# Kernel optimization log

Hardware: AMD Instinct MI355X
Metric: run time of the kernel (lower is better)

Reference implementation:

```python
import jax, jax.numpy as jnp
import numpy as np

T, B, DICO, EMB, LAT = 256, 64, 8192, 256, 256


def setup_inputs() -> dict:
    key = jax.random.key(0)
    ks = jax.random.split(key, 7)
    s_emb = 1.0 / np.sqrt(DICO)
    s_enc = 1.0 / np.sqrt(EMB + LAT)
    return {
        "x": jax.random.normal(ks[0], (T, B, DICO), dtype=jnp.float32),
        "h": jax.random.normal(ks[1], (B, LAT), dtype=jnp.float32),
        "W_emb": jax.random.uniform(ks[2], (DICO, EMB), jnp.float32, -s_emb, s_emb),
        "b_emb": jax.random.uniform(ks[3], (EMB,), jnp.float32, -s_emb, s_emb),
        "W_enc": jax.random.uniform(ks[4], (EMB + LAT, LAT), jnp.float32, -s_enc, s_enc),
        "b_enc": jax.random.uniform(ks[5], (LAT,), jnp.float32, -s_enc, s_enc),
    }


def reference(x, h, W_emb, b_emb, W_enc, b_enc):
    # embedding: [T,B,DICO] @ [DICO,EMB] -> [T,B,EMB]
    xe = jnp.einsum('tbd,de->tbe', x, W_emb) + b_emb
    # split encoder weight into x-part and h-part: cat(x,h)@W == x@Wx + h@Wh
    Wx, Wh = W_enc[:EMB], W_enc[EMB:]
    # hoist the per-step x projection out of the scan (no h dependence)
    xp = jnp.einsum('tbe,el->tbl', xe, Wx) + b_enc  # [T,B,LAT]

    def step(h, xp_t):
        h_new = jnp.tanh(xp_t + h @ Wh)
        return h_new, h_new

    _, hs = jax.lax.scan(step, h, xp)
    return hs  # [T,B,LAT]
```

## Files before the change

### kernel.cpp

```cpp
#include <hip/hip_runtime.h>
#include <hip/hip_bf16.h>
#include <stdint.h>

#define T_DIM 256
#define B_DIM 64
#define DICO  8192
#define EMB   256
#define LAT   256
#define M_DIM (T_DIM*B_DIM)

#define BM 64
#define BN 256
#define BK 64
#define KSPLIT 2
#define KCHUNK (DICO/KSPLIT)
#define NKS (KCHUNK/BK)

typedef short  bf16x8 __attribute__((ext_vector_type(8)));
typedef float  f32x4  __attribute__((ext_vector_type(4)));
typedef _Float16 f16x2 __attribute__((ext_vector_type(2)));

__device__ __forceinline__ ushort f2bf(float f) {
  uint32_t u = __float_as_uint(f);
  u += 0x7FFFu + ((u >> 16) & 1u);
  return (ushort)(u >> 16);
}

__device__ __forceinline__ void glds16(const void* g, void* l) {
  __builtin_amdgcn_global_load_lds(
      (const __attribute__((address_space(1))) uint32_t*)g,
      (__attribute__((address_space(3))) uint32_t*)l, 16, 0, 0);
}

__global__ void wct_kernel(const float* __restrict__ Wemb, const float* __restrict__ Wenc,
                           ushort* __restrict__ wct) {
  const int n  = threadIdx.x;
  const int d0 = blockIdx.x * 32;
  __shared__ float we[32 * 256];
  __shared__ float tr[32 * 257];
  #pragma unroll
  for (int r = 0; r < 32; ++r) we[r*256 + n] = Wemb[(size_t)(d0 + r)*EMB + n];
  __syncthreads();
  float acc[32];
  #pragma unroll
  for (int d = 0; d < 32; ++d) acc[d] = 0.f;
  #pragma unroll 4
  for (int e = 0; e < 256; ++e) {
    float wv = Wenc[e*LAT + n];
    #pragma unroll
    for (int d = 0; d < 32; ++d) acc[d] += we[d*256 + e] * wv;
  }
  #pragma unroll
  for (int d = 0; d < 32; ++d) tr[d*257 + n] = acc[d];
  __syncthreads();
  const int nn0 = n >> 2, kc = n & 3;
  #pragma unroll
  for (int p = 0; p < 4; ++p) {
    int nn = p*64 + nn0;
    bf16x8 v;
    #pragma unroll
    for (int j = 0; j < 8; ++j) v[j] = (short)f2bf(tr[(kc*8 + j)*257 + nn]);
    *(bf16x8*)(wct + (size_t)nn*DICO + d0 + kc*8) = v;
  }
}

__global__ void __launch_bounds__(256, 2) gemm_kernel(const float* __restrict__ x,
                                                      const ushort* __restrict__ wct,
                                                      float* __restrict__ xp) {
  __shared__ __align__(16) ushort sA[2][BM * BK];
  __shared__ __align__(16) ushort sB[2][BN * BK];
  const int tid = threadIdx.x;
  const int bid = blockIdx.x;
  const int swzb = (bid & 7) * 64 + (bid >> 3);
  const int mt = swzb & 255, ksp = swzb >> 8;
  const size_t rowbase = (size_t)mt * BM;
  const int kbase = ksp * KCHUNK;

  const int lane = tid & 63, wid = tid >> 6;
  const int l15 = lane & 15, lc = lane >> 4;

  const int r0 = tid >> 2, c0 = tid & 3;
  const float* ag = x + (rowbase + r0) * (size_t)DICO + kbase + c0 * 16;
  const int sx0 = (((2*c0    ) ^ (r0 & 7)) * 16);
  const int sx1 = (((2*c0 + 1) ^ (r0 & 7)) * 16);

  const int sw0 = (((    lc) ^ (l15 & 7)) * 16);
  const int sw1 = (((4 + lc) ^ (l15 & 7)) * 16);

  const char* wb = (const char*)wct;
  const size_t kb2 = (size_t)kbase * 2;

  const int brow_s = (tid >> 3);
  const int bslot_s = tid & 7;

  f32x4 acc[4][4];
  #pragma unroll
  for (int m = 0; m < 4; ++m)
    #pragma unroll
    for (int n = 0; n < 4; ++n) acc[m][n] = (f32x4){0.f, 0.f, 0.f, 0.f};

  float4 avP[4], avQ[4];

  auto stageB = [&](int buf, int kofs) {
    #pragma unroll
    for (int r = 0; r < 8; ++r) {
      const int row = r * 32 + brow_s;
      const int srcslot = bslot_s ^ (row & 7);
      glds16(wb + (size_t)row * (DICO * 2) + kb2 + (size_t)kofs * 2 + srcslot * 16,
             (char*)&sB[buf][0] + r * 4096 + tid * 16);
    }
  };
  auto storeA = [&](int buf, const float4* av) {
    const float4 a0 = av[0], a1 = av[1], a2 = av[2], a3 = av[3];
    bf16x8 w0, w1;
    w0[0]=(short)f2bf(a0.x); w0[1]=(short)f2bf(a0.y); w0[2]=(short)f2bf(a0.z); w0[3]=(short)f2bf(a0.w);
    w0[4]=(short)f2bf(a1.x); w0[5]=(short)f2bf(a1.y); w0[6]=(short)f2bf(a1.z); w0[7]=(short)f2bf(a1.w);
    w1[0]=(short)f2bf(a2.x); w1[1]=(short)f2bf(a2.y); w1[2]=(short)f2bf(a2.z); w1[3]=(short)f2bf(a2.w);
    w1[4]=(short)f2bf(a3.x); w1[5]=(short)f2bf(a3.y); w1[6]=(short)f2bf(a3.z); w1[7]=(short)f2bf(a3.w);
    char* base = (char*)&sA[buf][0] + r0 * 128;
    *(bf16x8*)(base + sx0) = w0;
    *(bf16x8*)(base + sx1) = w1;
  };
  auto compute = [&](int buf) {
    bf16x8 bfr[4][2];
    #pragma unroll
    for (int n = 0; n < 4; ++n) {
      const char* bb = (const char*)&sB[buf][0] + (wid*64 + n*16 + l15) * 128;
      bfr[n][0] = *(const bf16x8*)(bb + sw0);
      bfr[n][1] = *(const bf16x8*)(bb + sw1);
    }
    #pragma unroll
    for (int m = 0; m < 4; ++m) {
      const char* ab = (const char*)&sA[buf][0] + (m*16 + l15) * 128;
      bf16x8 a0 = *(const bf16x8*)(ab + sw0);
      bf16x8 a1 = *(const bf16x8*)(ab + sw1);
      #pragma unroll
      for (int n = 0; n < 4; ++n) {
        acc[m][n] = __builtin_amdgcn_mfma_f32_16x16x32_bf16(a0, bfr[n][0], acc[m][n], 0, 0, 0);
        acc[m][n] = __builtin_amdgcn_mfma_f32_16x16x32_bf16(a1, bfr[n][1], acc[m][n], 0, 0, 0);
      }
    }
  };

  auto body = [&](int k, float4* avC, float4* avL) {
    const int p = k & 1;
    const int kB = (k + 1 < NKS ? k + 1 : NKS - 1) * BK;
    const int kA = (k + 2 < NKS ? k + 2 : NKS - 1) * BK;
    stageB(p ^ 1, kB);
    asm volatile("" ::: "memory");
    #pragma unroll
    for (int q = 0; q < 4; ++q) avL[q] = *(const float4*)(ag + kA + q * 4);
    storeA(p ^ 1, avC);
    compute(p);
    asm volatile("s_waitcnt vmcnt(4)" ::: "memory");
    asm volatile("s_waitcnt lgkmcnt(0)" ::: "memory");
    __builtin_amdgcn_s_barrier();
    __builtin_amdgcn_sched_barrier(0);
  };

  stageB(0, 0);
  #pragma unroll
  for (int q = 0; q < 4; ++q) avP[q] = *(const float4*)(ag + 0   + q * 4);
  #pragma unroll
  for (int q = 0; q < 4; ++q) avQ[q] = *(const float4*)(ag + BK  + q * 4);
  storeA(0, avP);
  __syncthreads();

  for (int k = 0; k < NKS; k += 2) {
    body(k,     avQ, avP);
    body(k + 1, avP, avQ);
  }

  float* xpo = xp + ((size_t)ksp * M_DIM + rowbase) * LAT;
  #pragma unroll
  for (int m = 0; m < 4; ++m)
    #pragma unroll
    for (int n = 0; n < 4; ++n)
      #pragma unroll
      for (int j = 0; j < 4; ++j)
        xpo[(size_t)(m*16 + lc*4 + j) * LAT + wid*64 + n*16 + l15] = acc[m][n][j];
}

__global__ void __launch_bounds__(256, 1) rnn_kernel(const float* __restrict__ xp,
                           const float* __restrict__ h0, const float* __restrict__ Wenc,
                           const float* __restrict__ bemb, const float* __restrict__ benc,
                           float* __restrict__ out) {
  const int b = blockIdx.x, l = threadIdx.x;
  __shared__ __align__(16) uint32_t hbuf[2][128];
  float bc = benc[l];
  #pragma unroll 8
  for (int e = 0; e < 256; ++e) bc += bemb[e] * Wenc[e*LAT + l];
  f16x2 wh[128];
  #pragma unroll
  for (int j = 0; j < 128; ++j) {
    f16x2 w;
    w[0] = (_Float16)Wenc[(size_t)(EMB + 2*j    )*LAT + l];
    w[1] = (_Float16)Wenc[(size_t)(EMB + 2*j + 1)*LAT + l];
    wh[j] = w;
  }
  ((_Float16*)&hbuf[0][0])[l] = (_Float16)h0[(size_t)b*LAT + l];
  __syncthreads();
  const float* xpb = xp + (size_t)b*LAT + l;
  float*       ob  = out + (size_t)b*LAT + l;
  const size_t ST = (size_t)B_DIM * LAT;
  const size_t PO = (size_t)M_DIM * LAT;
  float xa0 = xpb[0],  xa1 = xpb[PO];
  float xb0 = xpb[ST], xb1 = xpb[ST + PO];
  float xc0 = 0.f, xc1 = 0.f;
  for (int t = 0; t < T_DIM; ++t) {
    if (t + 2 < T_DIM) {
      size_t ni = (size_t)(t + 2) * ST;
      xc0 = xpb[ni]; xc1 = xpb[ni + PO];
    }
    const uint32_t* hc = &hbuf[t & 1][0];
    float s0=0.f,s1=0.f,s2=0.f,s3=0.f,s4=0.f,s5=0.f,s6=0.f,s7=0.f;
    #pragma unroll
    for (int q = 0; q < 16; ++q) {
      uint4 hv0 = *(const uint4*)(hc + q*8);
      uint4 hv1 = *(const uint4*)(hc + q*8 + 4);
      s0 = __builtin_amdgcn_fdot2(wh[q*8+0], __builtin_bit_cast(f16x2, hv0.x), s0, false);
      s1 = __builtin_amdgcn_fdot2(wh[q*8+1], __builtin_bit_cast(f16x2, hv0.y), s1, false);
      s2 = __builtin_amdgcn_fdot2(wh[q*8+2], __builtin_bit_cast(f16x2, hv0.z), s2, false);
      s3 = __builtin_amdgcn_fdot2(wh[q*8+3], __builtin_bit_cast(f16x2, hv0.w), s3, false);
      s4 = __builtin_amdgcn_fdot2(wh[q*8+4], __builtin_bit_cast(f16x2, hv1.x), s4, false);
      s5 = __builtin_amdgcn_fdot2(wh[q*8+5], __builtin_bit_cast(f16x2, hv1.y), s5, false);
      s6 = __builtin_amdgcn_fdot2(wh[q*8+6], __builtin_bit_cast(f16x2, hv1.z), s6, false);
      s7 = __builtin_amdgcn_fdot2(wh[q*8+7], __builtin_bit_cast(f16x2, hv1.w), s7, false);
    }
    float pre = (xa0 + xa1) + bc + (((s0+s1)+(s2+s3)) + ((s4+s5)+(s6+s7)));
    float ax = fabsf(pre);
    float e2 = __expf(-2.f * ax);
    float r  = __fdividef(1.f - e2, 1.f + e2);
    float hn = (pre < 0.f) ? -r : r;
    ob[(size_t)t * ST] = hn;
    ((_Float16*)&hbuf[(t + 1) & 1][0])[l] = (_Float16)hn;
    __builtin_amdgcn_sched_barrier(0);
    asm volatile("s_waitcnt lgkmcnt(0)" ::: "memory");
    __builtin_amdgcn_s_barrier();
    __builtin_amdgcn_sched_barrier(0);
    xa0 = xb0; xa1 = xb1; xb0 = xc0; xb1 = xc1;
  }
}

extern "C" void kernel_launch(void* const* d_in, const int* in_sizes, int n_in,
                              void* d_out, int out_size, void* d_ws, size_t ws_size,
                              hipStream_t stream) {
  const float* x    = (const float*)d_in[0];
  const float* h0   = (const float*)d_in[1];
  const float* Wemb = (const float*)d_in[2];
  const float* bemb = (const float*)d_in[3];
  const float* Wenc = (const float*)d_in[4];
  const float* benc = (const float*)d_in[5];
  float* out = (float*)d_out;

  ushort* wct = (ushort*)d_ws;
  float*  xp  = (float*)((char*)d_ws + ((size_t)4 << 20));

  wct_kernel<<<256, 256, 0, stream>>>(Wemb, Wenc, wct);
  gemm_kernel<<<512, 256, 0, stream>>>(x, wct, xp);
  rnn_kernel<<<64, 256, 0, stream>>>(xp, h0, Wenc, bemb, benc, out);
}
```

Before: 658.9 us.

## Retile GEMM to 128x128 and move RNN recurrence onto MFMA

The input GEMM now uses 128x128 tiles with a 2x2 wave grid in place of 64x256, and converts fp32 to bf16 with the packed v_cvt_pk_bf16_f32 instruction. The recurrent kernel now computes 16 batch rows per block with fp16 MFMA instead of per-thread fdot2 dot products, running 4 blocks of 512 threads instead of 64 blocks. The RNN step becomes cheaper per block but uses far fewer CUs, so its latency depends on how serial steps run. The GEMM retiling changes how much of the x and weight data each tile reuses.

```diff
diff --git a/kernel.cpp b/kernel.cpp
--- a/kernel.cpp
+++ b/kernel.cpp
@@ -9,8 +9,6 @@
 #define LAT   256
 #define M_DIM (T_DIM*B_DIM)
 
-#define BM 64
-#define BN 256
 #define BK 64
 #define KSPLIT 2
 #define KCHUNK (DICO/KSPLIT)
@@ -18,12 +16,18 @@
 
 typedef short  bf16x8 __attribute__((ext_vector_type(8)));
 typedef float  f32x4  __attribute__((ext_vector_type(4)));
-typedef _Float16 f16x2 __attribute__((ext_vector_type(2)));
+typedef _Float16 f16x8 __attribute__((ext_vector_type(8)));
 
 __device__ __forceinline__ ushort f2bf(float f) {
   uint32_t u = __float_as_uint(f);
   u += 0x7FFFu + ((u >> 16) & 1u);
   return (ushort)(u >> 16);
+}
+
+__device__ __forceinline__ uint32_t cvtpk(float lo, float hi) {
+  uint32_t r;
+  asm("v_cvt_pk_bf16_f32 %0, %1, %2" : "=v"(r) : "v"(lo), "v"(hi));
+  return r;
 }
 
 __device__ __forceinline__ void glds16(const void* g, void* l) {
@@ -64,34 +68,36 @@
   }
 }
 
-__global__ void __launch_bounds__(256, 2) gemm_kernel(const float* __restrict__ x,
-                                                      const ushort* __restrict__ wct,
-                                                      float* __restrict__ xp) {
-  __shared__ __align__(16) ushort sA[2][BM * BK];
-  __shared__ __align__(16) ushort sB[2][BN * BK];
+__global__ void __launch_bounds__(256, 2) gemm2_kernel(const float* __restrict__ x,
+                                                       const ushort* __restrict__ wct,
+                                                       float* __restrict__ xp) {
+  __shared__ __align__(16) ushort sA[2][128 * 64];
+  __shared__ __align__(16) ushort sB[2][128 * 64];
   const int tid = threadIdx.x;
   const int bid = blockIdx.x;
   const int swzb = (bid & 7) * 64 + (bid >> 3);
-  const int mt = swzb & 255, ksp = swzb >> 8;
-  const size_t rowbase = (size_t)mt * BM;
+  const int mt  = swzb & 127;
+  const int nt  = (swzb >> 7) & 1;
+  const int ksp = swzb >> 8;
+  const size_t rowbase = (size_t)mt * 128;
   const int kbase = ksp * KCHUNK;
 
   const int lane = tid & 63, wid = tid >> 6;
   const int l15 = lane & 15, lc = lane >> 4;
-
-  const int r0 = tid >> 2, c0 = tid & 3;
-  const float* ag = x + (rowbase + r0) * (size_t)DICO + kbase + c0 * 16;
-  const int sx0 = (((2*c0    ) ^ (r0 & 7)) * 16);
-  const int sx1 = (((2*c0 + 1) ^ (r0 & 7)) * 16);
+  const int wr = wid >> 1, wc = wid & 1;
+
+  const int ar = tid >> 4, ac = tid & 15;
+  const float* ag = x + (rowbase + ar) * (size_t)DICO + kbase + ac * 4;
+  const int awb = (((ac >> 1) ^ (ar & 7)) * 16) + (ac & 1) * 8;
 
   const int sw0 = (((    lc) ^ (l15 & 7)) * 16);
   const int sw1 = (((4 + lc) ^ (l15 & 7)) * 16);
 
   const char* wb = (const char*)wct;
   const size_t kb2 = (size_t)kbase * 2;
-
-  const int brow_s = (tid >> 3);
-  const int bslot_s = tid & 7;
+  const int nrow0 = nt * 128;
+
+  const int brow_s = tid >> 3, bslot_s = tid & 7;
 
   f32x4 acc[4][4];
   #pragma unroll
@@ -99,39 +105,42 @@
     #pragma unroll
     for (int n = 0; n < 4; ++n) acc[m][n] = (f32x4){0.f, 0.f, 0.f, 0.f};
 
-  float4 avP[4], avQ[4];
-
+  float4 avP[8], avQ[8];
+
+  auto loadA = [&](float4* av, int kofs) {
+    #pragma unroll
+    for (int p = 0; p < 8; ++p)
+      av[p] = *(const float4*)(ag + (size_t)(p * 16) * DICO + kofs);
+  };
   auto stageB = [&](int buf, int kofs) {
     #pragma unroll
-    for (int r = 0; r < 8; ++r) {
+    for (int r = 0; r < 4; ++r) {
       const int row = r * 32 + brow_s;
       const int srcslot = bslot_s ^ (row & 7);
-      glds16(wb + (size_t)row * (DICO * 2) + kb2 + (size_t)kofs * 2 + srcslot * 16,
+      glds16(wb + (size_t)(nrow0 + row) * (DICO * 2) + kb2 + (size_t)kofs * 2 + srcslot * 16,
              (char*)&sB[buf][0] + r * 4096 + tid * 16);
     }
   };
   auto storeA = [&](int buf, const float4* av) {
-    const float4 a0 = av[0], a1 = av[1], a2 = av[2], a3 = av[3];
-    bf16x8 w0, w1;
-    w0[0]=(short)f2bf(a0.x); w0[1]=(short)f2bf(a0.y); w0[2]=(short)f2bf(a0.z); w0[3]=(short)f2bf(a0.w);
-    w0[4]=(short)f2bf(a1.x); w0[5]=(short)f2bf(a1.y); w0[6]=(short)f2bf(a1.z); w0[7]=(short)f2bf(a1.w);
-    w1[0]=(short)f2bf(a2.x); w1[1]=(short)f2bf(a2.y); w1[2]=(short)f2bf(a2.z); w1[3]=(short)f2bf(a2.w);
-    w1[4]=(short)f2bf(a3.x); w1[5]=(short)f2bf(a3.y); w1[6]=(short)f2bf(a3.z); w1[7]=(short)f2bf(a3.w);
-    char* base = (char*)&sA[buf][0] + r0 * 128;
-    *(bf16x8*)(base + sx0) = w0;
-    *(bf16x8*)(base + sx1) = w1;
+    #pragma unroll
+    for (int p = 0; p < 8; ++p) {
+      uint2 d;
+      d.x = cvtpk(av[p].x, av[p].y);
+      d.y = cvtpk(av[p].z, av[p].w);
+      *(uint2*)((char*)&sA[buf][0] + (p * 16 + ar) * 128 + awb) = d;
+    }
   };
   auto compute = [&](int buf) {
     bf16x8 bfr[4][2];
     #pragma unroll
     for (int n = 0; n < 4; ++n) {
-      const char* bb = (const char*)&sB[buf][0] + (wid*64 + n*16 + l15) * 128;
+      const char* bb = (const char*)&sB[buf][0] + (wc*64 + n*16 + l15) * 128;
       bfr[n][0] = *(const bf16x8*)(bb + sw0);
       bfr[n][1] = *(const bf16x8*)(bb + sw1);
     }
     #pragma unroll
     for (int m = 0; m < 4; ++m) {
-      const char* ab = (const char*)&sA[buf][0] + (m*16 + l15) * 128;
+      const char* ab = (const char*)&sA[buf][0] + (wr*64 + m*16 + l15) * 128;
       bf16x8 a0 = *(const bf16x8*)(ab + sw0);
       bf16x8 a1 = *(const bf16x8*)(ab + sw1);
       #pragma unroll
@@ -148,21 +157,21 @@
     const int kA = (k + 2 < NKS ? k + 2 : NKS - 1) * BK;
     stageB(p ^ 1, kB);
     asm volatile("" ::: "memory");
-    #pragma unroll
-    for (int q = 0; q < 4; ++q) avL[q] = *(const float4*)(ag + kA + q * 4);
+    loadA(avL, kA);
+    asm volatile("" ::: "memory");
     storeA(p ^ 1, avC);
     compute(p);
-    asm volatile("s_waitcnt vmcnt(4)" ::: "memory");
+    asm volatile("s_waitcnt vmcnt(8)" ::: "memory");
     asm volatile("s_waitcnt lgkmcnt(0)" ::: "memory");
     __builtin_amdgcn_s_barrier();
     __builtin_amdgcn_sched_barrier(0);
   };
 
   stageB(0, 0);
-  #pragma unroll
-  for (int q = 0; q < 4; ++q) avP[q] = *(const float4*)(ag + 0   + q * 4);
-  #pragma unroll
-  for (int q = 0; q < 4; ++q) avQ[q] = *(const float4*)(ag + BK  + q * 4);
+  asm volatile("" ::: "memory");
+  loadA(avP, 0);
+  asm volatile("" ::: "memory");
+  loadA(avQ, BK);
   storeA(0, avP);
   __syncthreads();
 
@@ -171,74 +180,107 @@
     body(k + 1, avP, avQ);
   }
 
-  float* xpo = xp + ((size_t)ksp * M_DIM + rowbase) * LAT;
+  float* xpo = xp + ((size_t)ksp * M_DIM + rowbase) * LAT + nrow0;
   #pragma unroll
   for (int m = 0; m < 4; ++m)
     #pragma unroll
     for (int n = 0; n < 4; ++n)
       #pragma unroll
       for (int j = 0; j < 4; ++j)
-        xpo[(size_t)(m*16 + lc*4 + j) * LAT + wid*64 + n*16 + l15] = acc[m][n][j];
-}
-
-__global__ void __launch_bounds__(256, 1) rnn_kernel(const float* __restrict__ xp,
+        xpo[(size_t)(wr*64 + m*16 + lc*4 + j) * LAT + wc*64 + n*16 + l15] = acc[m][n][j];
+}
+
+__global__ void __launch_bounds__(512, 2) rnn_mfma_kernel(const float* __restrict__ xp,
                            const float* __restrict__ h0, const float* __restrict__ Wenc,
                            const float* __restrict__ bemb, const float* __restrict__ benc,
                            float* __restrict__ out) {
-  const int b = blockIdx.x, l = threadIdx.x;
-  __shared__ __align__(16) uint32_t hbuf[2][128];
-  float bc = benc[l];
-  #pragma unroll 8
-  for (int e = 0; e < 256; ++e) bc += bemb[e] * Wenc[e*LAT + l];
-  f16x2 wh[128];
-  #pragma unroll
-  for (int j = 0; j < 128; ++j) {
-    f16x2 w;
-    w[0] = (_Float16)Wenc[(size_t)(EMB + 2*j    )*LAT + l];
-    w[1] = (_Float16)Wenc[(size_t)(EMB + 2*j + 1)*LAT + l];
-    wh[j] = w;
-  }
-  ((_Float16*)&hbuf[0][0])[l] = (_Float16)h0[(size_t)b*LAT + l];
+  const int tid = threadIdx.x;
+  const int w = tid >> 6, lane = tid & 63;
+  const int l15 = lane & 15, lc = lane >> 4;
+  const int bb = blockIdx.x * 16;
+  const int c0 = w*32 + l15, c1 = c0 + 16;
+  const int rb = lc * 4;
+
+  __shared__ _Float16 hbuf[2][16 * 264];
+
+  f16x8 whf0[8], whf1[8];
+  #pragma unroll
+  for (int ks = 0; ks < 8; ++ks) {
+    f16x8 w0, w1;
+    #pragma unroll
+    for (int j = 0; j < 8; ++j) {
+      const int k = ks*32 + lc*8 + j;
+      w0[j] = (_Float16)Wenc[(size_t)(EMB + k)*LAT + c0];
+      w1[j] = (_Float16)Wenc[(size_t)(EMB + k)*LAT + c1];
+    }
+    whf0[ks] = w0; whf1[ks] = w1;
+  }
+  float bc0 = benc[c0], bc1 = benc[c1];
+  for (int e = 0; e < 256; ++e) {
+    float be = bemb[e];
+    bc0 += be * Wenc[(size_t)e*LAT + c0];
+    bc1 += be * Wenc[(size_t)e*LAT + c1];
+  }
+  #pragma unroll
+  for (int j = 0; j < 4; ++j) {
+    hbuf[0][(rb + j)*264 + c0] = (_Float16)h0[(size_t)(bb + rb + j)*LAT + c0];
+    hbuf[0][(rb + j)*264 + c1] = (_Float16)h0[(size_t)(bb + rb + j)*LAT + c1];
+  }
   __syncthreads();
-  const float* xpb = xp + (size_t)b*LAT + l;
-  float*       ob  = out + (size_t)b*LAT + l;
-  const size_t ST = (size_t)B_DIM * LAT;
+
   const size_t PO = (size_t)M_DIM * LAT;
-  float xa0 = xpb[0],  xa1 = xpb[PO];
-  float xb0 = xpb[ST], xb1 = xpb[ST + PO];
-  float xc0 = 0.f, xc1 = 0.f;
-  for (int t = 0; t < T_DIM; ++t) {
-    if (t + 2 < T_DIM) {
-      size_t ni = (size_t)(t + 2) * ST;
-      xc0 = xpb[ni]; xc1 = xpb[ni + PO];
-    }
-    const uint32_t* hc = &hbuf[t & 1][0];
-    float s0=0.f,s1=0.f,s2=0.f,s3=0.f,s4=0.f,s5=0.f,s6=0.f,s7=0.f;
-    #pragma unroll
-    for (int q = 0; q < 16; ++q) {
-      uint4 hv0 = *(const uint4*)(hc + q*8);
-      uint4 hv1 = *(const uint4*)(hc + q*8 + 4);
-      s0 = __builtin_amdgcn_fdot2(wh[q*8+0], __builtin_bit_cast(f16x2, hv0.x), s0, false);
-      s1 = __builtin_amdgcn_fdot2(wh[q*8+1], __builtin_bit_cast(f16x2, hv0.y), s1, false);
-      s2 = __builtin_amdgcn_fdot2(wh[q*8+2], __builtin_bit_cast(f16x2, hv0.z), s2, false);
-      s3 = __builtin_amdgcn_fdot2(wh[q*8+3], __builtin_bit_cast(f16x2, hv0.w), s3, false);
-      s4 = __builtin_amdgcn_fdot2(wh[q*8+4], __builtin_bit_cast(f16x2, hv1.x), s4, false);
-      s5 = __builtin_amdgcn_fdot2(wh[q*8+5], __builtin_bit_cast(f16x2, hv1.y), s5, false);
-      s6 = __builtin_amdgcn_fdot2(wh[q*8+6], __builtin_bit_cast(f16x2, hv1.z), s6, false);
-      s7 = __builtin_amdgcn_fdot2(wh[q*8+7], __builtin_bit_cast(f16x2, hv1.w), s7, false);
-    }
-    float pre = (xa0 + xa1) + bc + (((s0+s1)+(s2+s3)) + ((s4+s5)+(s6+s7)));
-    float ax = fabsf(pre);
-    float e2 = __expf(-2.f * ax);
-    float r  = __fdividef(1.f - e2, 1.f + e2);
-    float hn = (pre < 0.f) ? -r : r;
-    ob[(size_t)t * ST] = hn;
-    ((_Float16*)&hbuf[(t + 1) & 1][0])[l] = (_Float16)hn;
+  float xpP[16], xpQ[16];
+  auto loadxp = [&](float* xb, int t) {
+    #pragma unroll
+    for (int j = 0; j < 4; ++j) {
+      const size_t m = ((size_t)t*B_DIM + bb + rb + j) * LAT;
+      xb[j*4 + 0] = xp[m + c0];
+      xb[j*4 + 1] = xp[m + c0 + PO];
+      xb[j*4 + 2] = xp[m + c1];
+      xb[j*4 + 3] = xp[m + c1 + PO];
+    }
+  };
+  loadxp(xpP, 0);
+  loadxp(xpQ, 1);
+
+  auto step = [&](int t, float* xb) {
+    const _Float16* hc = &hbuf[t & 1][0];
+    f32x4 acc0 = (f32x4){0.f,0.f,0.f,0.f};
+    f32x4 acc1 = (f32x4){0.f,0.f,0.f,0.f};
+    #pragma unroll
+    for (int ks = 0; ks < 8; ++ks) {
+      f16x8 a = *(const f16x8*)(hc + l15*264 + ks*32 + lc*8);
+      acc0 = __builtin_amdgcn_mfma_f32_16x16x32_f16(a, whf0[ks], acc0, 0, 0, 0);
+      acc1 = __builtin_amdgcn_mfma_f32_16x16x32_f16(a, whf1[ks], acc1, 0, 0, 0);
+    }
+    _Float16* hn_ = &hbuf[(t + 1) & 1][0];
+    float* ob = out + ((size_t)t*B_DIM + bb + rb) * LAT;
+    #pragma unroll
+    for (int j = 0; j < 4; ++j) {
+      float p0 = acc0[j] + bc0 + xb[j*4+0] + xb[j*4+1];
+      float p1 = acc1[j] + bc1 + xb[j*4+2] + xb[j*4+3];
+      float a0 = fabsf(p0),        a1 = fabsf(p1);
+      float e0 = __expf(-2.f*a0),  e1 = __expf(-2.f*a1);
+      float r0 = __fdividef(1.f - e0, 1.f + e0);
+      float r1 = __fdividef(1.f - e1, 1.f + e1);
+      float h0v = (p0 < 0.f) ? -r0 : r0;
+      float h1v = (p1 < 0.f) ? -r1 : r1;
+      ob[(size_t)j*LAT + c0] = h0v;
+      ob[(size_t)j*LAT + c1] = h1v;
+      hn_[(rb + j)*264 + c0] = (_Float16)h0v;
+      hn_[(rb + j)*264 + c1] = (_Float16)h1v;
+    }
+    const int tf = (t + 2 < T_DIM) ? t + 2 : T_DIM - 1;
+    loadxp(xb, tf);
     __builtin_amdgcn_sched_barrier(0);
     asm volatile("s_waitcnt lgkmcnt(0)" ::: "memory");
     __builtin_amdgcn_s_barrier();
     __builtin_amdgcn_sched_barrier(0);
-    xa0 = xb0; xa1 = xb1; xb0 = xc0; xb1 = xc1;
+  };
+
+  for (int t = 0; t < T_DIM; t += 2) {
+    step(t,     xpP);
+    step(t + 1, xpQ);
   }
 }
 
@@ -257,6 +299,6 @@
   float*  xp  = (float*)((char*)d_ws + ((size_t)4 << 20));
 
   wct_kernel<<<256, 256, 0, stream>>>(Wemb, Wenc, wct);
-  gemm_kernel<<<512, 256, 0, stream>>>(x, wct, xp);
-  rnn_kernel<<<64, 256, 0, stream>>>(xp, h0, Wenc, bemb, benc, out);
-}
+  gemm2_kernel<<<512, 256, 0, stream>>>(x, wct, xp);
+  rnn_mfma_kernel<<<4, 512, 0, stream>>>(xp, h0, Wenc, bemb, benc, out);
+}
```

Result: slower. 731.7 us (+11.0%).
